# Performance work log

Hardware: AMD Instinct MI355X
Metric: run time of the kernel (lower is better)

## Reference

```python
import jax, jax.numpy as jnp
import numpy as np

NSUB = 4  # fixed RK4 substeps per save interval (replaces diffrax adaptive stepping)


def _mlp(x, W0, b0, Wh, bh, Wo, bo, act, fact):
    h = act(W0 @ x + b0)
    for k in range(Wh.shape[0]):  # 3 stacked middle layers (static)
        h = act(Wh[k] @ h + bh[k])
    return fact(Wo @ h + bo)


def _forward(ts, ys, iW0, ib0, iWh, ibh, iWo, ibo, fW0, fb0, fWh, fbh, fWo, fbo, lW, lb):
    hid = iWo.shape[0]
    C = iW0.shape[1]  # in_size + 1 control channels

    def single(yseq):  # yseq: (T, obs)
        tys = jnp.concatenate([ts[:, None], yseq], axis=-1)  # (T, C)
        dts = ts[1:] - ts[:-1]                                # (T-1,)
        diffs = (tys[1:] - tys[:-1]) / dts[:, None]           # (T-1, C)
        # backward Hermite: deriv at t_i is backward difference, forward diff at t_0
        deriv = jnp.concatenate([diffs[:1], diffs], axis=0)   # (T, C)
        d0 = deriv[:-1]
        d1 = deriv[1:]
        c = (3.0 * diffs - 2.0 * d0 - d1) / dts[:, None]
        b = (d0 + d1 - 2.0 * diffs) / (dts * dts)[:, None]

        y0 = _mlp(tys[0], iW0, ib0, iWh, ibh, iWo, ibo, jax.nn.relu, lambda z: z)

        def vf(y):  # (hid, C)
            return _mlp(y, fW0, fb0, fWh, fbh, fWo, fbo, jax.nn.softplus, jnp.tanh).reshape(hid, C)

        def interval(y, xs):
            d0i, ci, bi, h = xs
            hs = h / NSUB

            def xdot(s):  # derivative of cubic Hermite control at local time s
                return d0i + 2.0 * ci * s + 3.0 * bi * s * s

            def f(s, yy):
                return vf(yy) @ xdot(s)

            def sub(k, yy):  # one RK4 substep
                s = k * hs
                k1 = f(s, yy)
                k2 = f(s + hs / 2, yy + hs / 2 * k1)
                k3 = f(s + hs / 2, yy + hs / 2 * k2)
                k4 = f(s + hs, yy + hs * k3)
                return yy + hs / 6 * (k1 + 2 * k2 + 2 * k3 + k4)

            y = jax.lax.fori_loop(0, NSUB, sub, y)
            return y, y

        _, ytail = jax.lax.scan(interval, y0, (d0, c, b, dts))
        ysol = jnp.concatenate([y0[None], ytail], axis=0)  # (T, hid)
        return ysol @ lW.T + lb                            # evolving_out readout

    return jax.vmap(single)(ys)


def setup_inputs() -> dict:
    key = jax.random.key(0)
    ks = jax.random.split(key, 10)
    T, B, obs, hid, width, out_size = 128, 64, 32, 64, 128, 32
    C = obs + 1
    fout = hid * C

    def lin(k, o, i):
        return jax.random.normal(k, (o, i), jnp.float32) / np.sqrt(i).astype(np.float32)

    return {
        "ts": jnp.arange(T, dtype=jnp.float32) / T,
        "ys": jax.random.normal(ks[0], (B, T, obs), jnp.float32) * 0.1,
        "iW0": lin(ks[1], width, C), "ib0": jnp.zeros((width,), jnp.float32),
        "iWh": jax.random.normal(ks[2], (3, width, width), jnp.float32) / np.sqrt(width).astype(np.float32),
        "ibh": jnp.zeros((3, width), jnp.float32),
        "iWo": lin(ks[3], hid, width), "ibo": jnp.zeros((hid,), jnp.float32),
        "fW0": lin(ks[4], width, hid), "fb0": jnp.zeros((width,), jnp.float32),
        "fWh": jax.random.normal(ks[5], (3, width, width), jnp.float32) / np.sqrt(width).astype(np.float32),
        "fbh": jnp.zeros((3, width), jnp.float32),
        "fWo": lin(ks[6], fout, width), "fbo": jnp.zeros((fout,), jnp.float32),
        "lW": lin(ks[7], out_size, hid), "lb": jnp.zeros((out_size,), jnp.float32),
    }


def reference(ts, ys, iW0, ib0, iWh, ibh, iWo, ibo, fW0, fb0, fWh, fbh, fWo, fbo, lW, lb):
    return _forward(ts, ys, iW0, ib0, iWh, ibh, iWo, ibo, fW0, fb0, fWh, fbh, fWo, fbo, lW, lb)
```

## Files before the change

kernel.cpp:

```cpp
#include <hip/hip_runtime.h>
#include <stdint.h>

#define T_N   128
#define B_N   64
#define OBS   32
#define C_N   33
#define HID   64
#define WID   128
#define FOUT  2112
#define OUTD  32
#define NSUB  4
#define NTH   1024

#define WS_PLANES 32
#define WS_NEED   ((size_t)WS_PLANES * NTH * 8 * 2)

__device__ __forceinline__ float b2f(unsigned short u) {
    return __uint_as_float(((unsigned int)u) << 16);
}
__device__ __forceinline__ float b2f_lo(unsigned int u) {
    return __uint_as_float(u << 16);
}
__device__ __forceinline__ float b2f_hi(unsigned int u) {
    return __uint_as_float(u & 0xffff0000u);
}
__device__ __forceinline__ unsigned short f2b(float f) {
    unsigned int u = __float_as_uint(f);
    unsigned int lsb = (u >> 16) & 1u;
    u += 0x7fffu + lsb;
    return (unsigned short)(u >> 16);
}
__device__ __forceinline__ unsigned int pack2(float a, float b) {
    return ((unsigned int)f2b(a)) | (((unsigned int)f2b(b)) << 16);
}
__device__ __forceinline__ float softplus_f(float x) {
    return fmaxf(x, 0.f) + __logf(1.f + __expf(-fabsf(x)));
}
__device__ __forceinline__ float tanh_fast(float x) {
    float e = __expf(2.f * x);
    return 1.f - 2.f / (e + 1.f);
}

struct PolBF16 {
    static __device__ __forceinline__ float ld(const void* p, int i) {
        return b2f(((const unsigned short*)p)[i]);
    }
    static __device__ __forceinline__ void ld8(const void* p, int i, float* o) {
        uint4 u = *(const uint4*)((const unsigned short*)p + i);
        o[0]=b2f_lo(u.x); o[1]=b2f_hi(u.x); o[2]=b2f_lo(u.y); o[3]=b2f_hi(u.y);
        o[4]=b2f_lo(u.z); o[5]=b2f_hi(u.z); o[6]=b2f_lo(u.w); o[7]=b2f_hi(u.w);
    }
    static __device__ __forceinline__ void st(void* p, int i, float v) {
        ((unsigned short*)p)[i] = f2b(v);
    }
};
struct PolF32 {
    static __device__ __forceinline__ float ld(const void* p, int i) {
        return ((const float*)p)[i];
    }
    static __device__ __forceinline__ void ld8(const void* p, int i, float* o) {
        const float4* q = (const float4*)((const float*)p + i);
        float4 a = q[0], b = q[1];
        o[0]=a.x; o[1]=a.y; o[2]=a.z; o[3]=a.w;
        o[4]=b.x; o[5]=b.y; o[6]=b.z; o[7]=b.w;
    }
    static __device__ __forceinline__ void st(void* p, int i, float v) {
        ((float*)p)[i] = v;
    }
};

struct __align__(16) Smem {
    uint4 whv[3][2][NTH];
    uint4 w0v[NTH];
    uint4 wxv[NTH];
    float h[2][WID];
    float y[HID];
    float yt[HID];
    float xd[C_N], d0[C_N], cc[C_N], bb[C_N];
    float fb0[WID];
    float fbh[3][WID];
    float lWt[HID*OUTD];
};

template<class P>
__device__ __forceinline__ void prep_body(const void* fWo, unsigned short* ws) {
    const int bid = blockIdx.x;
    const int tid = threadIdx.x;
    const int j    = bid >> 1;
    const int half = bid & 1;
    const int row  = (tid >> 4) * C_N + (tid & 15) + (half ? 16 : 0);
    float v[8];
    P::ld8(fWo, row*WID + j*8, v);
    uint4 u;
    u.x = pack2(v[0], v[1]); u.y = pack2(v[2], v[3]);
    u.z = pack2(v[4], v[5]); u.w = pack2(v[6], v[7]);
    ((uint4*)ws)[bid*NTH + tid] = u;
}
__global__ __launch_bounds__(NTH)
void prep_kernel(const void* ts, const void* fWo, unsigned short* ws) {
    const bool isbf = (((const unsigned short*)ts)[1] == 0x3C00);
    if (isbf) prep_body<PolBF16>(fWo, ws);
    else      prep_body<PolF32>(fWo, ws);
}

template<class P, bool COAL>
__device__ void run_cde(
    const void* ts, const void* ys, const void* iW0, const void* ib0,
    const void* iWh, const void* ibh, const void* iWo, const void* ibo,
    const void* fW0, const void* fb0, const void* fWh, const void* fbh,
    const void* fWo, const void* fbo, const void* lW, const void* lb,
    const void* wWo, void* out, Smem& S)
{
    const int tid  = threadIdx.x;
    const int b    = blockIdx.x;
    const int row8 = tid >> 3;
    const int seg8 = tid & 7;
    const int rot8 = seg8 >> 1;
    const int g16  = tid >> 4;
    const int l16  = tid & 15;
    const int r0   = g16*C_N + l16;
    const int r1   = r0 + 16;
    const int rx   = g16*C_N + 32;

    {
        const int kb = row8*HID + seg8*8;
        uint4 u;
        u.x = pack2(P::ld(fW0, kb+0), P::ld(fW0, kb+1));
        u.y = pack2(P::ld(fW0, kb+2), P::ld(fW0, kb+3));
        u.z = pack2(P::ld(fW0, kb+4), P::ld(fW0, kb+5));
        u.w = pack2(P::ld(fW0, kb+6), P::ld(fW0, kb+7));
        S.w0v[tid] = u;
    }
    #pragma unroll
    for (int l = 0; l < 3; ++l) {
        #pragma unroll
        for (int c = 0; c < 2; ++c) {
            const int j0 = (c*2 + 0 + rot8) & 3;
            const int j1 = (c*2 + 1 + rot8) & 3;
            const int k0 = (l*WID + row8)*WID + seg8*16 + j0*4;
            const int k1 = (l*WID + row8)*WID + seg8*16 + j1*4;
            uint4 u;
            u.x = pack2(P::ld(fWh, k0+0), P::ld(fWh, k0+1));
            u.y = pack2(P::ld(fWh, k0+2), P::ld(fWh, k0+3));
            u.z = pack2(P::ld(fWh, k1+0), P::ld(fWh, k1+1));
            u.w = pack2(P::ld(fWh, k1+2), P::ld(fWh, k1+3));
            S.whv[l][c][tid] = u;
        }
    }
    {
        const int kb = rx*WID + l16*8;
        uint4 u;
        u.x = pack2(P::ld(fWo, kb+0), P::ld(fWo, kb+1));
        u.y = pack2(P::ld(fWo, kb+2), P::ld(fWo, kb+3));
        u.z = pack2(P::ld(fWo, kb+4), P::ld(fWo, kb+5));
        u.w = pack2(P::ld(fWo, kb+6), P::ld(fWo, kb+7));
        S.wxv[tid] = u;
    }

    const float fb_r0 = P::ld(fbo, r0);
    const float fb_r1 = P::ld(fbo, r1);
    const float fb_rx = P::ld(fbo, rx);

    if (tid < WID)  S.fb0[tid] = P::ld(fb0, tid);
    if (tid < 3*WID) S.fbh[tid>>7][tid&127] = P::ld(fbh, tid);
    for (int i = tid; i < OUTD*HID; i += NTH) {
        int o = i >> 6, kk = i & 63;
        S.lWt[kk*OUTD + o] = P::ld(lW, i);
    }
    if (tid < C_N)
        S.xd[tid] = (tid == 0) ? P::ld(ts, 0) : P::ld(ys, b*T_N*OBS + (tid-1));
    __syncthreads();

    if (tid < WID) {
        float a = P::ld(ib0, tid);
        for (int k2 = 0; k2 < C_N; ++k2) a += P::ld(iW0, tid*C_N + k2) * S.xd[k2];
        S.h[0][tid] = fmaxf(a, 0.f);
    }
    __syncthreads();
    int pp = 0;
    for (int l = 0; l < 3; ++l) {
        if (tid < WID) {
            float a = P::ld(ibh, l*WID + tid);
            for (int k2 = 0; k2 < WID; ++k2)
                a += P::ld(iWh, (l*WID + tid)*WID + k2) * S.h[pp][k2];
            S.h[1-pp][tid] = fmaxf(a, 0.f);
        }
        __syncthreads();
        pp ^= 1;
    }
    if (tid < HID) {
        float a = P::ld(ibo, tid);
        for (int k2 = 0; k2 < WID; ++k2)
            a += P::ld(iWo, tid*WID + k2) * S.h[pp][k2];
        S.y[tid] = a;
    }
    __syncthreads();
    if (tid < OUTD) {
        float a = P::ld(lb, tid);
        for (int k2 = 0; k2 < HID; ++k2) a += S.lWt[k2*OUTD + tid] * S.y[k2];
        P::st(out, b*T_N*OUTD + tid, a);
    }

    #pragma unroll 1
    for (int iv = 0; iv < T_N-1; ++iv) {
        float t0 = P::ld(ts, iv), t1 = P::ld(ts, iv+1);
        float dt = t1 - t0;
        float hs = dt * (1.f/NSUB);
        if (tid < C_N) {
            float v0 = (tid==0) ? t0 : P::ld(ys, b*T_N*OBS + iv*OBS + (tid-1));
            float v1 = (tid==0) ? t1 : P::ld(ys, b*T_N*OBS + (iv+1)*OBS + (tid-1));
            float di = (v1 - v0) / dt;
            float d0v;
            if (iv == 0) d0v = di;
            else {
                float tm = P::ld(ts, iv-1);
                float vm = (tid==0) ? tm : P::ld(ys, b*T_N*OBS + (iv-1)*OBS + (tid-1));
                d0v = (v0 - vm) / (t0 - tm);
            }
            float d1v = di;
            S.d0[tid] = d0v;
            S.cc[tid] = (3.f*di - 2.f*d0v - d1v) / dt;
            S.bb[tid] = (d0v + d1v - 2.f*di) / (dt*dt);
        }
        __syncthreads();

        #pragma unroll 1
        for (int sub = 0; sub < NSUB; ++sub) {
            float s0 = sub * hs;
            float ka = 0.f, kb = 0.f, kc = 0.f;
            #pragma unroll 1
            for (int st = 0; st < 4; ++st) {
                float s = (st==0) ? s0 : ((st==3) ? s0+hs : s0 + 0.5f*hs);
                const float* yin = (st==0) ? S.y : S.yt;

                if (tid < C_N)
                    S.xd[tid] = S.d0[tid] + (2.f*S.cc[tid] + 3.f*S.bb[tid]*s)*s;

                {
                    const float4* y4 = (const float4*)(yin + seg8*8);
                    float4 ya = y4[0], yb = y4[1];
                    uint4 w = S.w0v[tid];
                    float a = b2f_lo(w.x)*ya.x + b2f_hi(w.x)*ya.y
                            + b2f_lo(w.y)*ya.z + b2f_hi(w.y)*ya.w
                            + b2f_lo(w.z)*yb.x + b2f_hi(w.z)*yb.y
                            + b2f_lo(w.w)*yb.z + b2f_hi(w.w)*yb.w;
                    a += __shfl_xor(a, 1);
                    a += __shfl_xor(a, 2);
                    a += __shfl_xor(a, 4);
                    if (seg8 == 0) S.h[0][row8] = softplus_f(a + S.fb0[row8]);
                }
                __syncthreads();

                #pragma unroll
                for (int l = 0; l < 3; ++l) {
                    const int hp = l & 1;
                    const float* hb = S.h[hp] + seg8*16;
                    uint4 wa = S.whv[l][0][tid];
                    uint4 wb = S.whv[l][1][tid];
                    float a;
                    { int j=(0+rot8)&3; float4 hv=*(const float4*)(hb+j*4);
                      a  = b2f_lo(wa.x)*hv.x + b2f_hi(wa.x)*hv.y
                         + b2f_lo(wa.y)*hv.z + b2f_hi(wa.y)*hv.w; }
                    { int j=(1+rot8)&3; float4 hv=*(const float4*)(hb+j*4);
                      a += b2f_lo(wa.z)*hv.x + b2f_hi(wa.z)*hv.y
                         + b2f_lo(wa.w)*hv.z + b2f_hi(wa.w)*hv.w; }
                    { int j=(2+rot8)&3; float4 hv=*(const float4*)(hb+j*4);
                      a += b2f_lo(wb.x)*hv.x + b2f_hi(wb.x)*hv.y
                         + b2f_lo(wb.y)*hv.z + b2f_hi(wb.y)*hv.w; }
                    { int j=(3+rot8)&3; float4 hv=*(const float4*)(hb+j*4);
                      a += b2f_lo(wb.z)*hv.x + b2f_hi(wb.z)*hv.y
                         + b2f_lo(wb.w)*hv.z + b2f_hi(wb.w)*hv.w; }
                    a += __shfl_xor(a, 1);
                    a += __shfl_xor(a, 2);
                    a += __shfl_xor(a, 4);
                    if (seg8 == 0) S.h[1-hp][row8] = softplus_f(a + S.fbh[l][row8]);
                    __syncthreads();
                }

                {
                    const float* hin = S.h[1];
                    float ax;
                    {
                        uint4 wxu = S.wxv[tid];
                        const float4* h4 = (const float4*)(hin + l16*8);
                        float4 ha = h4[0], hb2 = h4[1];
                        ax = b2f_lo(wxu.x)*ha.x + b2f_hi(wxu.x)*ha.y
                           + b2f_lo(wxu.y)*ha.z + b2f_hi(wxu.y)*ha.w
                           + b2f_lo(wxu.z)*hb2.x + b2f_hi(wxu.z)*hb2.y
                           + b2f_lo(wxu.w)*hb2.z + b2f_hi(wxu.w)*hb2.w;
                    }
                    float a0 = 0.f, a1 = 0.f;
                    if constexpr (COAL) {
                        const uint4* wp = (const uint4*)wWo + tid;
                        #pragma unroll 4
                        for (int j = 0; j < 16; ++j) {
                            const float4* h4 = (const float4*)(hin + j*8);
                            float4 ha = h4[0], hb2 = h4[1];
                            uint4 u0 = wp[(2*j+0)*NTH];
                            uint4 u1 = wp[(2*j+1)*NTH];
                            a0 += b2f_lo(u0.x)*ha.x + b2f_hi(u0.x)*ha.y
                                + b2f_lo(u0.y)*ha.z + b2f_hi(u0.y)*ha.w
                                + b2f_lo(u0.z)*hb2.x + b2f_hi(u0.z)*hb2.y
                                + b2f_lo(u0.w)*hb2.z + b2f_hi(u0.w)*hb2.w;
                            a1 += b2f_lo(u1.x)*ha.x + b2f_hi(u1.x)*ha.y
                                + b2f_lo(u1.y)*ha.z + b2f_hi(u1.y)*ha.w
                                + b2f_lo(u1.z)*hb2.x + b2f_hi(u1.z)*hb2.y
                                + b2f_lo(u1.w)*hb2.z + b2f_hi(u1.w)*hb2.w;
                        }
                    } else {
                        #pragma unroll 4
                        for (int j = 0; j < 16; ++j) {
                            const float4* h4 = (const float4*)(hin + j*8);
                            float4 ha = h4[0], hb2 = h4[1];
                            float w8[8];
                            P::ld8(fWo, r0*WID + j*8, w8);
                            a0 += w8[0]*ha.x + w8[1]*ha.y + w8[2]*ha.z + w8[3]*ha.w
                                + w8[4]*hb2.x + w8[5]*hb2.y + w8[6]*hb2.z + w8[7]*hb2.w;
                            P::ld8(fWo, r1*WID + j*8, w8);
                            a1 += w8[0]*ha.x + w8[1]*ha.y + w8[2]*ha.z + w8[3]*ha.w
                                + w8[4]*hb2.x + w8[5]*hb2.y + w8[6]*hb2.z + w8[7]*hb2.w;
                        }
                    }
                    ax += __shfl_xor(ax, 1);
                    ax += __shfl_xor(ax, 2);
                    ax += __shfl_xor(ax, 4);
                    ax += __shfl_xor(ax, 8);

                    float v0 = tanh_fast(a0 + fb_r0) * S.xd[l16];
                    float v1 = tanh_fast(a1 + fb_r1) * S.xd[16 + l16];
                    float t2 = v0 + v1;
                    t2 += __shfl_xor(t2, 1);
                    t2 += __shfl_xor(t2, 2);
                    t2 += __shfl_xor(t2, 4);
                    t2 += __shfl_xor(t2, 8);
                    float ksum = t2 + tanh_fast(ax + fb_rx) * S.xd[32];

                    if (l16 == 0) {
                        float yg = S.y[g16];
                        if (st == 0)      { ka = ksum; S.yt[g16] = yg + 0.5f*hs*ksum; }
                        else if (st == 1) { kb = ksum; S.yt[g16] = yg + 0.5f*hs*ksum; }
                        else if (st == 2) { kc = ksum; S.yt[g16] = yg + hs*ksum; }
                        else S.y[g16] = yg + hs*(1.f/6.f)*(ka + 2.f*kb + 2.f*kc + ksum);
                    }
                }
                __syncthreads();
            }
        }

        if (tid < OUTD) {
            float a = P::ld(lb, tid);
            #pragma unroll 8
            for (int k2 = 0; k2 < HID; ++k2) a += S.lWt[k2*OUTD + tid] * S.y[k2];
            P::st(out, b*T_N*OUTD + (iv+1)*OUTD + tid, a);
        }
    }
}

__global__ __launch_bounds__(NTH)
void cde_kernel(const void* ts, const void* ys, const void* iW0, const void* ib0,
                const void* iWh, const void* ibh, const void* iWo, const void* ibo,
                const void* fW0, const void* fb0, const void* fWh, const void* fbh,
                const void* fWo, const void* fbo, const void* lW, const void* lb,
                const unsigned short* ws, int use_ws, void* out)
{
    __shared__ Smem S;
    const bool isbf = (((const unsigned short*)ts)[1] == 0x3C00);
    if (use_ws) {
        if (isbf)
            run_cde<PolBF16, true>(ts, ys, iW0, ib0, iWh, ibh, iWo, ibo,
                                   fW0, fb0, fWh, fbh, fWo, fbo, lW, lb,
                                   ws, out, S);
        else
            run_cde<PolF32, true>(ts, ys, iW0, ib0, iWh, ibh, iWo, ibo,
                                  fW0, fb0, fWh, fbh, fWo, fbo, lW, lb,
                                  ws, out, S);
    } else {
        if (isbf)
            run_cde<PolBF16, false>(ts, ys, iW0, ib0, iWh, ibh, iWo, ibo,
                                    fW0, fb0, fWh, fbh, fWo, fbo, lW, lb,
                                    fWo, out, S);
        else
            run_cde<PolF32, false>(ts, ys, iW0, ib0, iWh, ibh, iWo, ibo,
                                   fW0, fb0, fWh, fbh, fWo, fbo, lW, lb,
                                   fWo, out, S);
    }
}

extern "C" void kernel_launch(void* const* d_in, const int* in_sizes, int n_in,
                              void* d_out, int out_size, void* d_ws, size_t ws_size,
                              hipStream_t stream) {
    (void)in_sizes; (void)n_in; (void)out_size;
    const int use_ws = (ws_size >= WS_NEED) ? 1 : 0;
    if (use_ws) {
        hipLaunchKernelGGL(prep_kernel, dim3(WS_PLANES), dim3(NTH), 0, stream,
                           d_in[0], d_in[12], (unsigned short*)d_ws);
    }
    hipLaunchKernelGGL(cde_kernel, dim3(B_N), dim3(NTH), 0, stream,
                       d_in[0], d_in[1], d_in[2], d_in[3], d_in[4], d_in[5],
                       d_in[6], d_in[7], d_in[8], d_in[9], d_in[10], d_in[11],
                       d_in[12], d_in[13], d_in[14], d_in[15],
                       (const unsigned short*)d_ws, use_ws, d_out);
}
```

Before: 13.53 ms.

## Compute vector-field output layer with bf16 MFMA tiles over a repacked weight workspace

Replaces the per-thread scalar dot products for the 2112x128 output layer with MFMA 16x16x32 bf16 instructions. Each wave loops over 16-row tiles of the weights, which a prep kernel repacks into MFMA operand layout. The hidden activation is split into high and low bf16 parts so the matrix unit keeps near-fp32 accuracy for that operand. Partial sums from two K halves go through shared memory and an extra barrier before the tanh and contraction step. This trades the scalar FMA and shuffle work for matrix-unit throughput, at the cost of doubled MFMA issues, a pipelined global load per tile, and more shared-memory traffic.

```diff
diff --git a/kernel.cpp b/kernel.cpp
--- a/kernel.cpp
+++ b/kernel.cpp
@@ -12,8 +12,12 @@
 #define NSUB  4
 #define NTH   1024
 
-#define WS_PLANES 32
-#define WS_NEED   ((size_t)WS_PLANES * NTH * 8 * 2)
+#define NTILE_T  132
+#define NPLANES  (NTILE_T*4)
+#define WS_NEED  ((size_t)NPLANES * 64 * 16)
+
+typedef __attribute__((ext_vector_type(8))) short  bf16x8;
+typedef __attribute__((ext_vector_type(4))) float  f32x4;
 
 __device__ __forceinline__ float b2f(unsigned short u) {
     return __uint_as_float(((unsigned int)u) << 16);
@@ -33,6 +37,17 @@
 __device__ __forceinline__ unsigned int pack2(float a, float b) {
     return ((unsigned int)f2b(a)) | (((unsigned int)f2b(b)) << 16);
 }
+__device__ __forceinline__ unsigned int pkhi(float a, float b) {
+    return (__float_as_uint(a) >> 16) | (__float_as_uint(b) & 0xffff0000u);
+}
+__device__ __forceinline__ unsigned int pklo(float a, float b) {
+    float la = a - __uint_as_float(__float_as_uint(a) & 0xffff0000u);
+    float lb = b - __uint_as_float(__float_as_uint(b) & 0xffff0000u);
+    return pack2(la, lb);
+}
+__device__ __forceinline__ bf16x8 u4b8(uint4 u) {
+    union { uint4 a; bf16x8 b; } x; x.a = u; return x.b;
+}
 __device__ __forceinline__ float softplus_f(float x) {
     return fmaxf(x, 0.f) + __logf(1.f + __expf(-fabsf(x)));
 }
@@ -72,7 +87,7 @@
 struct __align__(16) Smem {
     uint4 whv[3][2][NTH];
     uint4 w0v[NTH];
-    uint4 wxv[NTH];
+    float rowp[2][FOUT];
     float h[2][WID];
     float y[HID];
     float yt[HID];
@@ -84,17 +99,19 @@
 
 template<class P>
 __device__ __forceinline__ void prep_body(const void* fWo, unsigned short* ws) {
-    const int bid = blockIdx.x;
-    const int tid = threadIdx.x;
-    const int j    = bid >> 1;
-    const int half = bid & 1;
-    const int row  = (tid >> 4) * C_N + (tid & 15) + (half ? 16 : 0);
+    const int e    = blockIdx.x * NTH + threadIdx.x;
+    const int p    = e >> 6;
+    const int lane = e & 63;
+    const int t    = p >> 2;
+    const int kb   = p & 3;
+    const int row  = 16*t + (lane & 15);
+    const int k0   = kb*32 + ((lane >> 4) << 3);
     float v[8];
-    P::ld8(fWo, row*WID + j*8, v);
+    P::ld8(fWo, row*WID + k0, v);
     uint4 u;
-    u.x = pack2(v[0], v[1]); u.y = pack2(v[2], v[3]);
-    u.z = pack2(v[4], v[5]); u.w = pack2(v[6], v[7]);
-    ((uint4*)ws)[bid*NTH + tid] = u;
+    u.x = pack2(v[0],v[1]); u.y = pack2(v[2],v[3]);
+    u.z = pack2(v[4],v[5]); u.w = pack2(v[6],v[7]);
+    ((uint4*)ws)[e] = u;
 }
 __global__ __launch_bounds__(NTH)
 void prep_kernel(const void* ts, const void* fWo, unsigned short* ws) {
@@ -121,6 +138,11 @@
     const int r0   = g16*C_N + l16;
     const int r1   = r0 + 16;
     const int rx   = g16*C_N + 32;
+    const int wv   = tid >> 6;
+    const int lane = tid & 63;
+    const int pr   = wv & 7;
+    const int role = wv >> 3;
+    const int lg   = lane >> 4;
 
     {
         const int kb = row8*HID + seg8*8;
@@ -146,15 +168,6 @@
             u.w = pack2(P::ld(fWh, k1+2), P::ld(fWh, k1+3));
             S.whv[l][c][tid] = u;
         }
-    }
-    {
-        const int kb = rx*WID + l16*8;
-        uint4 u;
-        u.x = pack2(P::ld(fWo, kb+0), P::ld(fWo, kb+1));
-        u.y = pack2(P::ld(fWo, kb+2), P::ld(fWo, kb+3));
-        u.z = pack2(P::ld(fWo, kb+4), P::ld(fWo, kb+5));
-        u.w = pack2(P::ld(fWo, kb+6), P::ld(fWo, kb+7));
-        S.wxv[tid] = u;
     }
 
     const float fb_r0 = P::ld(fbo, r0);
@@ -277,55 +290,102 @@
                     __syncthreads();
                 }
 
-                {
-                    const float* hin = S.h[1];
-                    float ax;
+                const float* hin = S.h[1];
+                if constexpr (COAL) {
+                    const int kbse = role*64 + lg*8;
+                    float4 p0 = *(const float4*)(hin + kbse);
+                    float4 p1 = *(const float4*)(hin + kbse + 4);
+                    float4 p2 = *(const float4*)(hin + kbse + 32);
+                    float4 p3 = *(const float4*)(hin + kbse + 36);
+                    uint4 bh0, bl0, bh1, bl1;
+                    bh0.x=pkhi(p0.x,p0.y); bh0.y=pkhi(p0.z,p0.w);
+                    bh0.z=pkhi(p1.x,p1.y); bh0.w=pkhi(p1.z,p1.w);
+                    bl0.x=pklo(p0.x,p0.y); bl0.y=pklo(p0.z,p0.w);
+                    bl0.z=pklo(p1.x,p1.y); bl0.w=pklo(p1.z,p1.w);
+                    bh1.x=pkhi(p2.x,p2.y); bh1.y=pkhi(p2.z,p2.w);
+                    bh1.z=pkhi(p3.x,p3.y); bh1.w=pkhi(p3.z,p3.w);
+                    bl1.x=pklo(p2.x,p2.y); bl1.y=pklo(p2.z,p2.w);
+                    bl1.z=pklo(p3.x,p3.y); bl1.w=pklo(p3.z,p3.w);
+                    bf16x8 vh0=u4b8(bh0), vl0=u4b8(bl0);
+                    bf16x8 vh1=u4b8(bh1), vl1=u4b8(bl1);
+
+                    const uint4* ap = (const uint4*)wWo
+                                    + (pr*4 + 2*role)*64 + lane;
+                    const int ntile = (pr < 4) ? 17 : 16;
+                    uint4 a0 = ap[0], a1 = ap[64];
+                    int t = pr;
+                    #pragma unroll 1
+                    for (int i = 0; i < ntile; ++i) {
+                        uint4 c0 = a0, c1 = a1;
+                        if (i + 1 < ntile) {
+                            ap += 8*4*64;
+                            a0 = ap[0]; a1 = ap[64];
+                        }
+                        f32x4 acc = {0.f, 0.f, 0.f, 0.f};
+                        acc = __builtin_amdgcn_mfma_f32_16x16x32_bf16(
+                                  u4b8(c0), vh0, acc, 0, 0, 0);
+                        acc = __builtin_amdgcn_mfma_f32_16x16x32_bf16(
+                                  u4b8(c0), vl0, acc, 0, 0, 0);
+                        acc = __builtin_amdgcn_mfma_f32_16x16x32_bf16(
+                                  u4b8(c1), vh1, acc, 0, 0, 0);
+                        acc = __builtin_amdgcn_mfma_f32_16x16x32_bf16(
+                                  u4b8(c1), vl1, acc, 0, 0, 0);
+                        if ((lane & 15) == 0) {
+                            float4 st4;
+                            st4.x = acc[0]; st4.y = acc[1];
+                            st4.z = acc[2]; st4.w = acc[3];
+                            *(float4*)&S.rowp[role][16*t + lg*4] = st4;
+                        }
+                        t += 8;
+                    }
+                    __syncthreads();
+
                     {
-                        uint4 wxu = S.wxv[tid];
+                        float d0v = S.rowp[0][r0] + S.rowp[1][r0];
+                        float d1v = S.rowp[0][r1] + S.rowp[1][r1];
+                        float dxv = S.rowp[0][rx] + S.rowp[1][rx];
+                        float v0 = tanh_fast(d0v + fb_r0) * S.xd[l16];
+                        float v1 = tanh_fast(d1v + fb_r1) * S.xd[16 + l16];
+                        float t2 = v0 + v1;
+                        t2 += __shfl_xor(t2, 1);
+                        t2 += __shfl_xor(t2, 2);
+                        t2 += __shfl_xor(t2, 4);
+                        t2 += __shfl_xor(t2, 8);
+                        float ksum = t2 + tanh_fast(dxv + fb_rx) * S.xd[32];
+                        if (l16 == 0) {
+                            float yg = S.y[g16];
+                            if (st == 0)      { ka = ksum; S.yt[g16] = yg + 0.5f*hs*ksum; }
+                            else if (st == 1) { kb = ksum; S.yt[g16] = yg + 0.5f*hs*ksum; }
+                            else if (st == 2) { kc = ksum; S.yt[g16] = yg + hs*ksum; }
+                            else S.y[g16] = yg + hs*(1.f/6.f)*(ka + 2.f*kb + 2.f*kc + ksum);
+                        }
+                    }
+                } else {
+                    float a0 = 0.f, a1 = 0.f, ax = 0.f;
+                    #pragma unroll 2
+                    for (int j = 0; j < 16; ++j) {
+                        const float4* h4 = (const float4*)(hin + j*8);
+                        float4 ha = h4[0], hb2 = h4[1];
+                        float w8[8];
+                        P::ld8(fWo, r0*WID + j*8, w8);
+                        a0 += w8[0]*ha.x + w8[1]*ha.y + w8[2]*ha.z + w8[3]*ha.w
+                            + w8[4]*hb2.x + w8[5]*hb2.y + w8[6]*hb2.z + w8[7]*hb2.w;
+                        P::ld8(fWo, r1*WID + j*8, w8);
+                        a1 += w8[0]*ha.x + w8[1]*ha.y + w8[2]*ha.z + w8[3]*ha.w
+                            + w8[4]*hb2.x + w8[5]*hb2.y + w8[6]*hb2.z + w8[7]*hb2.w;
+                    }
+                    {
+                        float w8[8];
+                        P::ld8(fWo, rx*WID + l16*8, w8);
                         const float4* h4 = (const float4*)(hin + l16*8);
                         float4 ha = h4[0], hb2 = h4[1];
-                        ax = b2f_lo(wxu.x)*ha.x + b2f_hi(wxu.x)*ha.y
-                           + b2f_lo(wxu.y)*ha.z + b2f_hi(wxu.y)*ha.w
-                           + b2f_lo(wxu.z)*hb2.x + b2f_hi(wxu.z)*hb2.y
-                           + b2f_lo(wxu.w)*hb2.z + b2f_hi(wxu.w)*hb2.w;
-                    }
-                    float a0 = 0.f, a1 = 0.f;
-                    if constexpr (COAL) {
-                        const uint4* wp = (const uint4*)wWo + tid;
-                        #pragma unroll 4
-                        for (int j = 0; j < 16; ++j) {
-                            const float4* h4 = (const float4*)(hin + j*8);
-                            float4 ha = h4[0], hb2 = h4[1];
-                            uint4 u0 = wp[(2*j+0)*NTH];
-                            uint4 u1 = wp[(2*j+1)*NTH];
-                            a0 += b2f_lo(u0.x)*ha.x + b2f_hi(u0.x)*ha.y
-                                + b2f_lo(u0.y)*ha.z + b2f_hi(u0.y)*ha.w
-                                + b2f_lo(u0.z)*hb2.x + b2f_hi(u0.z)*hb2.y
-                                + b2f_lo(u0.w)*hb2.z + b2f_hi(u0.w)*hb2.w;
-                            a1 += b2f_lo(u1.x)*ha.x + b2f_hi(u1.x)*ha.y
-                                + b2f_lo(u1.y)*ha.z + b2f_hi(u1.y)*ha.w
-                                + b2f_lo(u1.z)*hb2.x + b2f_hi(u1.z)*hb2.y
-                                + b2f_lo(u1.w)*hb2.z + b2f_hi(u1.w)*hb2.w;
-                        }
-                    } else {
-                        #pragma unroll 4
-                        for (int j = 0; j < 16; ++j) {
-                            const float4* h4 = (const float4*)(hin + j*8);
-                            float4 ha = h4[0], hb2 = h4[1];
-                            float w8[8];
-                            P::ld8(fWo, r0*WID + j*8, w8);
-                            a0 += w8[0]*ha.x + w8[1]*ha.y + w8[2]*ha.z + w8[3]*ha.w
-                                + w8[4]*hb2.x + w8[5]*hb2.y + w8[6]*hb2.z + w8[7]*hb2.w;
-                            P::ld8(fWo, r1*WID + j*8, w8);
-                            a1 += w8[0]*ha.x + w8[1]*ha.y + w8[2]*ha.z + w8[3]*ha.w
-                                + w8[4]*hb2.x + w8[5]*hb2.y + w8[6]*hb2.z + w8[7]*hb2.w;
-                        }
+                        ax = w8[0]*ha.x + w8[1]*ha.y + w8[2]*ha.z + w8[3]*ha.w
+                           + w8[4]*hb2.x + w8[5]*hb2.y + w8[6]*hb2.z + w8[7]*hb2.w;
                     }
                     ax += __shfl_xor(ax, 1);
                     ax += __shfl_xor(ax, 2);
                     ax += __shfl_xor(ax, 4);
                     ax += __shfl_xor(ax, 8);
-
                     float v0 = tanh_fast(a0 + fb_r0) * S.xd[l16];
                     float v1 = tanh_fast(a1 + fb_r1) * S.xd[16 + l16];
                     float t2 = v0 + v1;
@@ -334,7 +394,6 @@
                     t2 += __shfl_xor(t2, 4);
                     t2 += __shfl_xor(t2, 8);
                     float ksum = t2 + tanh_fast(ax + fb_rx) * S.xd[32];
-
                     if (l16 == 0) {
                         float yg = S.y[g16];
                         if (st == 0)      { ka = ksum; S.yt[g16] = yg + 0.5f*hs*ksum; }
@@ -392,7 +451,8 @@
     (void)in_sizes; (void)n_in; (void)out_size;
     const int use_ws = (ws_size >= WS_NEED) ? 1 : 0;
     if (use_ws) {
-        hipLaunchKernelGGL(prep_kernel, dim3(WS_PLANES), dim3(NTH), 0, stream,
+        const int nprep = (NPLANES * 64) / NTH;
+        hipLaunchKernelGGL(prep_kernel, dim3(nprep), dim3(NTH), 0, stream,
                            d_in[0], d_in[12], (unsigned short*)d_ws);
     }
     hipLaunchKernelGGL(cde_kernel, dim3(B_N), dim3(NTH), 0, stream,
```

New measurement: 13.93 ms. +2.9%, slower.

## Use packed f32x2 FMA for bf16 dot products and keep small weights in registers

Applied to the files above, without the earlier changes.

Rewrites the bf16-weight dot products in the vector-field MLP as two-wide float vector multiply-adds, so the compiler can emit packed FP32 FMA instructions on the MI355X. It also moves the first-layer and extra-output-row weight tiles out of shared memory into per-thread registers, dropping two LDS reads per stage. The cost is higher register pressure in a 1024-thread block, and the split accumulators change the floating-point summation order slightly.

```diff
diff --git a/kernel.cpp b/kernel.cpp
--- a/kernel.cpp
+++ b/kernel.cpp
@@ -13,7 +13,10 @@
 #define NTH   1024
 
 #define WS_PLANES 32
-#define WS_NEED   ((size_t)WS_PLANES * NTH * 8 * 2)
+#define PLB       (NTH * 16)
+#define WS_NEED   ((size_t)WS_PLANES * PLB)
+
+typedef __attribute__((ext_vector_type(2))) float f32x2;
 
 __device__ __forceinline__ float b2f(unsigned short u) {
     return __uint_as_float(((unsigned int)u) << 16);
@@ -40,6 +43,12 @@
     float e = __expf(2.f * x);
     return 1.f - 2.f / (e + 1.f);
 }
+__device__ __forceinline__ f32x2 up2(unsigned int u) {
+    f32x2 r; r.x = b2f_lo(u); r.y = b2f_hi(u); return r;
+}
+__device__ __forceinline__ f32x2 mk2(float a, float b) {
+    f32x2 r; r.x = a; r.y = b; return r;
+}
 
 struct PolBF16 {
     static __device__ __forceinline__ float ld(const void* p, int i) {
@@ -71,8 +80,6 @@
 
 struct __align__(16) Smem {
     uint4 whv[3][2][NTH];
-    uint4 w0v[NTH];
-    uint4 wxv[NTH];
     float h[2][WID];
     float y[HID];
     float yt[HID];
@@ -122,15 +129,23 @@
     const int r1   = r0 + 16;
     const int rx   = g16*C_N + 32;
 
+    uint4 w0v;
     {
         const int kb = row8*HID + seg8*8;
-        uint4 u;
-        u.x = pack2(P::ld(fW0, kb+0), P::ld(fW0, kb+1));
-        u.y = pack2(P::ld(fW0, kb+2), P::ld(fW0, kb+3));
-        u.z = pack2(P::ld(fW0, kb+4), P::ld(fW0, kb+5));
-        u.w = pack2(P::ld(fW0, kb+6), P::ld(fW0, kb+7));
-        S.w0v[tid] = u;
-    }
+        w0v.x = pack2(P::ld(fW0, kb+0), P::ld(fW0, kb+1));
+        w0v.y = pack2(P::ld(fW0, kb+2), P::ld(fW0, kb+3));
+        w0v.z = pack2(P::ld(fW0, kb+4), P::ld(fW0, kb+5));
+        w0v.w = pack2(P::ld(fW0, kb+6), P::ld(fW0, kb+7));
+    }
+    uint4 wxv;
+    {
+        const int kb = rx*WID + l16*8;
+        wxv.x = pack2(P::ld(fWo, kb+0), P::ld(fWo, kb+1));
+        wxv.y = pack2(P::ld(fWo, kb+2), P::ld(fWo, kb+3));
+        wxv.z = pack2(P::ld(fWo, kb+4), P::ld(fWo, kb+5));
+        wxv.w = pack2(P::ld(fWo, kb+6), P::ld(fWo, kb+7));
+    }
+
     #pragma unroll
     for (int l = 0; l < 3; ++l) {
         #pragma unroll
@@ -146,15 +161,6 @@
             u.w = pack2(P::ld(fWh, k1+2), P::ld(fWh, k1+3));
             S.whv[l][c][tid] = u;
         }
-    }
-    {
-        const int kb = rx*WID + l16*8;
-        uint4 u;
-        u.x = pack2(P::ld(fWo, kb+0), P::ld(fWo, kb+1));
-        u.y = pack2(P::ld(fWo, kb+2), P::ld(fWo, kb+3));
-        u.z = pack2(P::ld(fWo, kb+4), P::ld(fWo, kb+5));
-        u.w = pack2(P::ld(fWo, kb+6), P::ld(fWo, kb+7));
-        S.wxv[tid] = u;
     }
 
     const float fb_r0 = P::ld(fbo, r0);
@@ -239,11 +245,12 @@
                 {
                     const float4* y4 = (const float4*)(yin + seg8*8);
                     float4 ya = y4[0], yb = y4[1];
-                    uint4 w = S.w0v[tid];
-                    float a = b2f_lo(w.x)*ya.x + b2f_hi(w.x)*ya.y
-                            + b2f_lo(w.y)*ya.z + b2f_hi(w.y)*ya.w
-                            + b2f_lo(w.z)*yb.x + b2f_hi(w.z)*yb.y
-                            + b2f_lo(w.w)*yb.z + b2f_hi(w.w)*yb.w;
+                    f32x2 av = {0.f, 0.f};
+                    av += up2(w0v.x) * mk2(ya.x, ya.y);
+                    av += up2(w0v.y) * mk2(ya.z, ya.w);
+                    av += up2(w0v.z) * mk2(yb.x, yb.y);
+                    av += up2(w0v.w) * mk2(yb.z, yb.w);
+                    float a = av.x + av.y;
                     a += __shfl_xor(a, 1);
                     a += __shfl_xor(a, 2);
                     a += __shfl_xor(a, 4);
@@ -257,19 +264,20 @@
                     const float* hb = S.h[hp] + seg8*16;
                     uint4 wa = S.whv[l][0][tid];
                     uint4 wb = S.whv[l][1][tid];
-                    float a;
+                    f32x2 av = {0.f, 0.f};
                     { int j=(0+rot8)&3; float4 hv=*(const float4*)(hb+j*4);
-                      a  = b2f_lo(wa.x)*hv.x + b2f_hi(wa.x)*hv.y
-                         + b2f_lo(wa.y)*hv.z + b2f_hi(wa.y)*hv.w; }
+                      av += up2(wa.x)*mk2(hv.x,hv.y);
+                      av += up2(wa.y)*mk2(hv.z,hv.w); }
                     { int j=(1+rot8)&3; float4 hv=*(const float4*)(hb+j*4);
-                      a += b2f_lo(wa.z)*hv.x + b2f_hi(wa.z)*hv.y
-                         + b2f_lo(wa.w)*hv.z + b2f_hi(wa.w)*hv.w; }
+                      av += up2(wa.z)*mk2(hv.x,hv.y);
+                      av += up2(wa.w)*mk2(hv.z,hv.w); }
                     { int j=(2+rot8)&3; float4 hv=*(const float4*)(hb+j*4);
-                      a += b2f_lo(wb.x)*hv.x + b2f_hi(wb.x)*hv.y
-                         + b2f_lo(wb.y)*hv.z + b2f_hi(wb.y)*hv.w; }
+                      av += up2(wb.x)*mk2(hv.x,hv.y);
+                      av += up2(wb.y)*mk2(hv.z,hv.w); }
                     { int j=(3+rot8)&3; float4 hv=*(const float4*)(hb+j*4);
-                      a += b2f_lo(wb.z)*hv.x + b2f_hi(wb.z)*hv.y
-                         + b2f_lo(wb.w)*hv.z + b2f_hi(wb.w)*hv.w; }
+                      av += up2(wb.z)*mk2(hv.x,hv.y);
+                      av += up2(wb.w)*mk2(hv.z,hv.w); }
+                    float a = av.x + av.y;
                     a += __shfl_xor(a, 1);
                     a += __shfl_xor(a, 2);
                     a += __shfl_xor(a, 4);
@@ -279,17 +287,16 @@
 
                 {
                     const float* hin = S.h[1];
-                    float ax;
+                    f32x2 AX = {0.f, 0.f};
                     {
-                        uint4 wxu = S.wxv[tid];
                         const float4* h4 = (const float4*)(hin + l16*8);
                         float4 ha = h4[0], hb2 = h4[1];
-                        ax = b2f_lo(wxu.x)*ha.x + b2f_hi(wxu.x)*ha.y
-                           + b2f_lo(wxu.y)*ha.z + b2f_hi(wxu.y)*ha.w
-                           + b2f_lo(wxu.z)*hb2.x + b2f_hi(wxu.z)*hb2.y
-                           + b2f_lo(wxu.w)*hb2.z + b2f_hi(wxu.w)*hb2.w;
+                        AX += up2(wxv.x) * mk2(ha.x, ha.y);
+                        AX += up2(wxv.y) * mk2(ha.z, ha.w);
+                        AX += up2(wxv.z) * mk2(hb2.x, hb2.y);
+                        AX += up2(wxv.w) * mk2(hb2.z, hb2.w);
                     }
-                    float a0 = 0.f, a1 = 0.f;
+                    f32x2 A0 = {0.f, 0.f}, A1 = {0.f, 0.f};
                     if constexpr (COAL) {
                         const uint4* wp = (const uint4*)wWo + tid;
                         #pragma unroll 4
@@ -298,14 +305,12 @@
                             float4 ha = h4[0], hb2 = h4[1];
                             uint4 u0 = wp[(2*j+0)*NTH];
                             uint4 u1 = wp[(2*j+1)*NTH];
-                            a0 += b2f_lo(u0.x)*ha.x + b2f_hi(u0.x)*ha.y
-                                + b2f_lo(u0.y)*ha.z + b2f_hi(u0.y)*ha.w
-                                + b2f_lo(u0.z)*hb2.x + b2f_hi(u0.z)*hb2.y
-                                + b2f_lo(u0.w)*hb2.z + b2f_hi(u0.w)*hb2.w;
-                            a1 += b2f_lo(u1.x)*ha.x + b2f_hi(u1.x)*ha.y
-                                + b2f_lo(u1.y)*ha.z + b2f_hi(u1.y)*ha.w
-                                + b2f_lo(u1.z)*hb2.x + b2f_hi(u1.z)*hb2.y
-                                + b2f_lo(u1.w)*hb2.z + b2f_hi(u1.w)*hb2.w;
+                            f32x2 h01 = mk2(ha.x, ha.y),  h23 = mk2(ha.z, ha.w);
+                            f32x2 h45 = mk2(hb2.x,hb2.y), h67 = mk2(hb2.z,hb2.w);
+                            A0 += up2(u0.x)*h01; A0 += up2(u0.y)*h23;
+                            A0 += up2(u0.z)*h45; A0 += up2(u0.w)*h67;
+                            A1 += up2(u1.x)*h01; A1 += up2(u1.y)*h23;
+                            A1 += up2(u1.z)*h45; A1 += up2(u1.w)*h67;
                         }
                     } else {
                         #pragma unroll 4
@@ -313,14 +318,19 @@
                             const float4* h4 = (const float4*)(hin + j*8);
                             float4 ha = h4[0], hb2 = h4[1];
                             float w8[8];
+                            f32x2 h01 = mk2(ha.x, ha.y),  h23 = mk2(ha.z, ha.w);
+                            f32x2 h45 = mk2(hb2.x,hb2.y), h67 = mk2(hb2.z,hb2.w);
                             P::ld8(fWo, r0*WID + j*8, w8);
-                            a0 += w8[0]*ha.x + w8[1]*ha.y + w8[2]*ha.z + w8[3]*ha.w
-                                + w8[4]*hb2.x + w8[5]*hb2.y + w8[6]*hb2.z + w8[7]*hb2.w;
+                            A0 += mk2(w8[0],w8[1])*h01; A0 += mk2(w8[2],w8[3])*h23;
+                            A0 += mk2(w8[4],w8[5])*h45; A0 += mk2(w8[6],w8[7])*h67;
                             P::ld8(fWo, r1*WID + j*8, w8);
-                            a1 += w8[0]*ha.x + w8[1]*ha.y + w8[2]*ha.z + w8[3]*ha.w
-                                + w8[4]*hb2.x + w8[5]*hb2.y + w8[6]*hb2.z + w8[7]*hb2.w;
+                            A1 += mk2(w8[0],w8[1])*h01; A1 += mk2(w8[2],w8[3])*h23;
+                            A1 += mk2(w8[4],w8[5])*h45; A1 += mk2(w8[6],w8[7])*h67;
                         }
                     }
+                    float a0 = A0.x + A0.y;
+                    float a1 = A1.x + A1.y;
+                    float ax = AX.x + AX.y;
                     ax += __shfl_xor(ax, 1);
                     ax += __shfl_xor(ax, 2);
                     ax += __shfl_xor(ax, 4);
```

Result: no change. 13.33 ms, median of 2 (-1.5%).
